# Kernel optimization log

Hardware: AMD Instinct MI355X
Metric: run time of the kernel (lower is better)

Reference implementation:

```python
import jax, jax.numpy as jnp
import numpy as np

N_NODES = 100000
N_EDGES = 1600000
D_IN = 128
D_OUT = 128
NEG_SLOPE = 0.01  # torch F.leaky_relu default


def setup_inputs() -> dict:
    key = jax.random.key(0)
    k1, k2, k3, k4, k5 = jax.random.split(key, 5)
    h = jax.random.normal(k1, (N_NODES, D_IN), dtype=jnp.float32)
    # nn.Linear default init scale ~ 1/sqrt(fan_in)
    W = jax.random.normal(k2, (D_IN, D_OUT), dtype=jnp.float32) / np.sqrt(D_IN)
    attn_w = jax.random.normal(k3, (2 * D_OUT,), dtype=jnp.float32) / np.sqrt(2 * D_OUT)
    edge_src = jax.random.randint(k4, (N_EDGES,), 0, N_NODES, dtype=jnp.int32)
    edge_dst = jax.random.randint(k5, (N_EDGES,), 0, N_NODES, dtype=jnp.int32)
    return {"h": h, "W": W, "attn_w": attn_w, "edge_src": edge_src, "edge_dst": edge_dst}


def reference(h, W, attn_w, edge_src, edge_dst):
    n = h.shape[0]
    d = W.shape[1]
    z = h @ W                                   # [N, d]
    # attention_func(cat([z_src, z_dst])) == z_src @ a[:d] + z_dst @ a[d:]
    s_src = z @ attn_w[:d]                      # [N]
    s_dst = z @ attn_w[d:]                      # [N]
    e = jax.nn.leaky_relu(s_src[edge_src] + s_dst[edge_dst], NEG_SLOPE)  # [E]
    # segment softmax over incoming edges of each dst node
    m = jax.ops.segment_max(e, edge_dst, num_segments=n)   # [N], -inf for empty
    ex = jnp.exp(e - m[edge_dst])                           # [E]
    denom = jax.ops.segment_sum(ex, edge_dst, num_segments=n)  # [N]
    alpha = ex / denom[edge_dst]                             # [E]
    # weighted neighbor sum: sum_j alpha_ij * z_j
    out = jax.ops.segment_sum(alpha[:, None] * z[edge_src], edge_dst, num_segments=n)
    return out
```

## Files before the change

kernel.cpp:

```cpp
#include <hip/hip_runtime.h>

#define D 128
#define NEG_SLOPE 0.01f
#define BSHIFT 7
#define B1 1024
#define SCHUNK 4096
#define SLOT 2560

typedef __attribute__((ext_vector_type(8))) short short8;
typedef __attribute__((ext_vector_type(4))) float floatx4;

__device__ __forceinline__ unsigned f2bf_rne(float x) {
    unsigned u = __float_as_uint(x);
    return (u + 0x7fffu + ((u >> 16) & 1u)) >> 16;
}
#define BF_LO(u) __uint_as_float((u) << 16)
#define BF_HI(u) __uint_as_float((u) & 0xffff0000u)

__global__ __launch_bounds__(256) void prep_wfrag(const float* __restrict__ W,
                                                  unsigned short* __restrict__ whi,
                                                  unsigned short* __restrict__ wlo,
                                                  int* __restrict__ gcur) {
    if (blockIdx.x == 0) {
        for (int i = threadIdx.x; i < B1; i += 256) gcur[i] = i * SLOT;
    }
    const int idx = blockIdx.x * 256 + threadIdx.x;
    const int j    = idx & 7;
    const int lane = (idx >> 3) & 63;
    const int tk   = idx >> 9;
    const int kk = tk & 3, ct = tk >> 2;
    const int k = kk * 32 + (lane >> 4) * 8 + j;
    const int n = ct * 16 + (lane & 15);
    const float x = W[k * D + n];
    const unsigned hi = f2bf_rne(x);
    const float hf = __uint_as_float(hi << 16);
    whi[idx] = (unsigned short)hi;
    wlo[idx] = (unsigned short)(__float_as_uint(x - hf) >> 16);
}

__global__ __launch_bounds__(1024) void sort_scatter(const int* __restrict__ esrc,
                                                     const int* __restrict__ edst,
                                                     int* __restrict__ gcur,
                                                     int* __restrict__ pairs, int E) {
    __shared__ int cnt[B1], exc[B1], gbs[B1], cur[B1];
    __shared__ int spk[SCHUNK];
    __shared__ unsigned short sbkt[SCHUNK];
    __shared__ int wtot[16];
    const int t = threadIdx.x;
    const int lane = t & 63, wv = t >> 6;
    cnt[t] = 0; cur[t] = 0;
    __syncthreads();

    const int e0 = blockIdx.x * SCHUNK;
    const int n  = min(SCHUNK, E - e0);

    int pk[4], bk[4];
    const int i0 = t * 4;
    if (i0 + 3 < n) {
        const int4 dv = *(const int4*)&edst[e0 + i0];
        const int4 sv = *(const int4*)&esrc[e0 + i0];
        const int dd[4] = {dv.x, dv.y, dv.z, dv.w};
        const int ss[4] = {sv.x, sv.y, sv.z, sv.w};
#pragma unroll
        for (int k = 0; k < 4; ++k) {
            bk[k] = dd[k] >> BSHIFT;
            pk[k] = (ss[k] << BSHIFT) | (dd[k] & 127);
            atomicAdd(&cnt[bk[k]], 1);
        }
    } else {
#pragma unroll
        for (int k = 0; k < 4; ++k) {
            const int i = i0 + k;
            if (i < n) {
                const int d = edst[e0 + i];
                const int s = esrc[e0 + i];
                bk[k] = d >> BSHIFT;
                pk[k] = (s << BSHIFT) | (d & 127);
                atomicAdd(&cnt[bk[k]], 1);
            } else {
                bk[k] = -1;
            }
        }
    }
    __syncthreads();

    const int c = cnt[t];
    int incl = c;
#pragma unroll
    for (int o = 1; o < 64; o <<= 1) {
        int v = __shfl_up(incl, o, 64);
        if (lane >= o) incl += v;
    }
    if (lane == 63) wtot[wv] = incl;
    __syncthreads();
    int wpre = 0;
#pragma unroll
    for (int i = 0; i < 16; ++i) wpre += (i < wv) ? wtot[i] : 0;
    exc[t] = wpre + incl - c;
    if (c > 0) gbs[t] = atomicAdd(&gcur[t], c);
    __syncthreads();

#pragma unroll
    for (int k = 0; k < 4; ++k) {
        if (bk[k] >= 0) {
            const int p = exc[bk[k]] + atomicAdd(&cur[bk[k]], 1);
            spk[p]  = pk[k];
            sbkt[p] = (unsigned short)bk[k];
        }
    }
    __syncthreads();

    for (int i = t; i < n; i += 1024) {
        const int b = sbkt[i];
        const int pos = gbs[b] + (i - exc[b]);
        if (pos < (b + 1) * SLOT) pairs[pos] = spk[i];
    }
}

__global__ __launch_bounds__(256) void fine_build(const int* __restrict__ pairs,
                                                  const int* __restrict__ gcur,
                                                  int* __restrict__ beg,
                                                  int* __restrict__ ncnt,
                                                  int* __restrict__ adj, int N) {
    __shared__ int cnt[4][128], woff[4][128], cur[4][128];
    __shared__ int sc[128];
    const int b = blockIdx.x;
    const int base = b << BSHIFT;
    const int nd = min(128, N - base);
    const int t = threadIdx.x;
    const int wv = t >> 6;
    const int s0 = b * SLOT;
    const int e1 = min(gcur[b], s0 + SLOT);
    for (int i = t; i < 512; i += 256) { (&cnt[0][0])[i] = 0; (&cur[0][0])[i] = 0; }
    __syncthreads();
    for (int i = s0 + t; i < e1; i += 256)
        atomicAdd(&cnt[wv][pairs[i] & 127], 1);
    __syncthreads();
    if (t < 128) {
        const int c0 = cnt[0][t], c1 = cnt[1][t], c2 = cnt[2][t];
        woff[0][t] = 0; woff[1][t] = c0; woff[2][t] = c0 + c1; woff[3][t] = c0 + c1 + c2;
        sc[t] = c0 + c1 + c2 + cnt[3][t];
    }
    __syncthreads();
    for (int off = 1; off < 128; off <<= 1) {
        int v = (t < 128 && t >= off) ? sc[t - off] : 0;
        __syncthreads();
        if (t < 128) sc[t] += v;
        __syncthreads();
    }
    if (t < 128) {
        const int tot = cnt[0][t] + cnt[1][t] + cnt[2][t] + cnt[3][t];
        const int excl = sc[t] - tot;
        if (t < nd) { beg[base + t] = s0 + excl; ncnt[base + t] = tot; }
        woff[0][t] += excl; woff[1][t] += excl; woff[2][t] += excl; woff[3][t] += excl;
    }
    __syncthreads();
    for (int i = s0 + t; i < e1; i += 256) {
        const int pkv = pairs[i];
        const int d = pkv & 127;
        const int pos = s0 + woff[wv][d] + atomicAdd(&cur[wv][d], 1);
        adj[pos] = pkv >> BSHIFT;
    }
}

__global__ __launch_bounds__(256, 3) void gemm_zs(const float* __restrict__ h,
                                                  const unsigned short* __restrict__ whi,
                                                  const unsigned short* __restrict__ wlo,
                                                  const float* __restrict__ aw,
                                                  unsigned short* __restrict__ z,
                                                  float* __restrict__ s_src,
                                                  float* __restrict__ s_dst, int N) {
    const int t = threadIdx.x;
    const int lane = t & 63, quad = lane >> 4, l16 = lane & 15;
    const int rowbase = blockIdx.x * 64 + (t >> 6) * 16;
    const int arow = min(rowbase + l16, N - 1);
    const float* __restrict__ hrow = h + (size_t)arow * D;

    float4 hx[8];
#pragma unroll
    for (int kk = 0; kk < 4; ++kk) {
        const int k0 = kk * 32 + quad * 8;
        hx[kk * 2]     = *(const float4*)&hrow[k0];
        hx[kk * 2 + 1] = *(const float4*)&hrow[k0 + 4];
    }
    union { short8 v; unsigned short u[8]; } ahi[4], alo[4];
#pragma unroll
    for (int kk = 0; kk < 4; ++kk) {
        const float xs[8] = {hx[kk*2].x, hx[kk*2].y, hx[kk*2].z, hx[kk*2].w,
                             hx[kk*2+1].x, hx[kk*2+1].y, hx[kk*2+1].z, hx[kk*2+1].w};
#pragma unroll
        for (int i = 0; i < 8; ++i) {
            const unsigned hi = f2bf_rne(xs[i]);
            const float hf = __uint_as_float(hi << 16);
            ahi[kk].u[i] = (unsigned short)hi;
            alo[kk].u[i] = (unsigned short)(__float_as_uint(xs[i] - hf) >> 16);
        }
    }

    floatx4 acc[8];
#pragma unroll
    for (int ct = 0; ct < 8; ++ct) acc[ct] = (floatx4){0.f, 0.f, 0.f, 0.f};

#pragma unroll
    for (int kk = 0; kk < 4; ++kk)
#pragma unroll
        for (int ct = 0; ct < 8; ++ct) {
            const int fo = ((ct * 4 + kk) * 64 + lane) * 8;
            short8 bhi = *(const short8*)&whi[fo];
            short8 blo = *(const short8*)&wlo[fo];
            acc[ct] = __builtin_amdgcn_mfma_f32_16x16x32_bf16(ahi[kk].v, bhi, acc[ct], 0, 0, 0);
            acc[ct] = __builtin_amdgcn_mfma_f32_16x16x32_bf16(alo[kk].v, bhi, acc[ct], 0, 0, 0);
            acc[ct] = __builtin_amdgcn_mfma_f32_16x16x32_bf16(ahi[kk].v, blo, acc[ct], 0, 0, 0);
        }

#pragma unroll
    for (int ct = 0; ct < 8; ++ct)
#pragma unroll
        for (int reg = 0; reg < 4; ++reg) {
            int r = rowbase + quad * 4 + reg;
            if (r < N)
                z[(size_t)r * D + ct * 16 + l16] = (unsigned short)f2bf_rne(acc[ct][reg]);
        }

    float ps[4] = {0.f, 0.f, 0.f, 0.f}, pd[4] = {0.f, 0.f, 0.f, 0.f};
#pragma unroll
    for (int ct = 0; ct < 8; ++ct) {
        float as = aw[ct * 16 + l16];
        float ad = aw[128 + ct * 16 + l16];
#pragma unroll
        for (int reg = 0; reg < 4; ++reg) {
            ps[reg] = fmaf(acc[ct][reg], as, ps[reg]);
            pd[reg] = fmaf(acc[ct][reg], ad, pd[reg]);
        }
    }
#pragma unroll
    for (int reg = 0; reg < 4; ++reg)
#pragma unroll
        for (int o = 1; o < 16; o <<= 1) {
            ps[reg] += __shfl_xor(ps[reg], o, 64);
            pd[reg] += __shfl_xor(pd[reg], o, 64);
        }
    if (l16 == 0) {
#pragma unroll
        for (int reg = 0; reg < 4; ++reg) {
            int r = rowbase + quad * 4 + reg;
            if (r < N) { s_src[r] = ps[reg]; s_dst[r] = pd[reg]; }
        }
    }
}

__global__ __launch_bounds__(256) void aggregate(const unsigned short* __restrict__ z,
                                                 const float* __restrict__ s_src,
                                                 const float* __restrict__ s_dst,
                                                 const int* __restrict__ beg_,
                                                 const int* __restrict__ ncnt_,
                                                 const int* __restrict__ adj,
                                                 float* __restrict__ out, int N) {
    const int lane = threadIdx.x & 63;
    const int half = lane >> 5;
    const int l32  = lane & 31;
    const int q2   = l32 >> 4;
    const int l16  = lane & 15;
    const int hb   = half << 5;
    const int pairBase = blockIdx.x * 8 + (threadIdx.x >> 6) * 2;
    if (pairBase >= N) return;
    const int nodeA = pairBase, nodeB = pairBase + 1;
    const int cA = ncnt_[nodeA], bA = beg_[nodeA];
    int cB = 0, bB = 0;
    if (nodeB < N) { cB = ncnt_[nodeB]; bB = beg_[nodeB]; }

    auto fma8 = [&](float* ac, float w, const uint4& v) {
        ac[0] = fmaf(w, BF_LO(v.x), ac[0]); ac[1] = fmaf(w, BF_HI(v.x), ac[1]);
        ac[2] = fmaf(w, BF_LO(v.y), ac[2]); ac[3] = fmaf(w, BF_HI(v.y), ac[3]);
        ac[4] = fmaf(w, BF_LO(v.z), ac[4]); ac[5] = fmaf(w, BF_HI(v.z), ac[5]);
        ac[6] = fmaf(w, BF_LO(v.w), ac[6]); ac[7] = fmaf(w, BF_HI(v.w), ac[7]);
    };

    if (max(cA, cB) <= 32) {
        const int myn = pairBase + half;
        const int mb  = half ? bB : bA;
        const int mc  = half ? cB : cA;
        const float sd = s_dst[myn < N ? myn : 0];
        int s = 0; float e = -INFINITY;
        if (l32 < mc) {
            s = adj[mb + l32];
            float tt = s_src[s] + sd;
            e = (tt >= 0.f) ? tt : NEG_SLOPE * tt;
        }
        int sj[4]; uint4 zv[4];
#pragma unroll
        for (int u = 0; u < 4; ++u) sj[u] = __shfl(s, hb + u * 2 + q2, 64);
#pragma unroll
        for (int u = 0; u < 4; ++u)
            zv[u] = *(const uint4*)&z[(size_t)sj[u] * D + l16 * 8];

        float mx = e;
#pragma unroll
        for (int o = 16; o; o >>= 1) mx = fmaxf(mx, __shfl_xor(mx, o, 64));
        float ex = (l32 < mc) ? __expf(e - mx) : 0.f;
        float sum = ex;
#pragma unroll
        for (int o = 16; o; o >>= 1) sum += __shfl_xor(sum, o, 64);
        const float inv = (mc > 0) ? 1.f / sum : 0.f;
        const float w = ex * inv;

        float a[8] = {0.f,0.f,0.f,0.f,0.f,0.f,0.f,0.f};
        float bacc[8] = {0.f,0.f,0.f,0.f,0.f,0.f,0.f,0.f};
#pragma unroll
        for (int u = 0; u < 4; ++u) {
            const int ji = u * 2 + q2;
            float wj = __shfl(w, hb + ji, 64);
            wj = (ji < mc) ? wj : 0.f;
            fma8((u & 1) ? bacc : a, wj, zv[u]);
        }
        for (int jj = 8; jj < mc; jj += 8) {
            int ji2[4]; float wj[4]; int sj2[4];
#pragma unroll
            for (int u = 0; u < 4; ++u) {
                ji2[u] = jj + u * 2 + q2;
                wj[u]  = __shfl(w, hb + ji2[u], 64);
                sj2[u] = __shfl(s, hb + ji2[u], 64);
                wj[u]  = (ji2[u] < mc) ? wj[u] : 0.f;
            }
            uint4 z0 = *(const uint4*)&z[(size_t)sj2[0] * D + l16 * 8];
            uint4 z1 = *(const uint4*)&z[(size_t)sj2[1] * D + l16 * 8];
            uint4 z2 = *(const uint4*)&z[(size_t)sj2[2] * D + l16 * 8];
            uint4 z3 = *(const uint4*)&z[(size_t)sj2[3] * D + l16 * 8];
            fma8(a, wj[0], z0);
            fma8(bacc, wj[1], z1);
            fma8(a, wj[2], z2);
            fma8(bacc, wj[3], z3);
        }
#pragma unroll
        for (int i = 0; i < 8; ++i) {
            a[i] += bacc[i];
            a[i] += __shfl_xor(a[i], 16, 64);
        }
        if (q2 == 0 && myn < N) {
            float* o = &out[(size_t)myn * D + l16 * 8];
            *(float4*)o       = make_float4(a[0], a[1], a[2], a[3]);
            *(float4*)(o + 4) = make_float4(a[4], a[5], a[6], a[7]);
        }
        return;
    }

    const int q = lane >> 4;
    for (int which = 0; which < 2; ++which) {
        const int myn = which ? nodeB : nodeA;
        if (myn >= N) break;
        const int mb = which ? bB : bA;
        const int mc = which ? cB : cA;
        const float sd = s_dst[myn];
        float a[8] = {0.f,0.f,0.f,0.f,0.f,0.f,0.f,0.f};
        float bacc[8] = {0.f,0.f,0.f,0.f,0.f,0.f,0.f,0.f};
        float mx = -INFINITY;
        for (int j = lane; j < mc; j += 64) {
            float tt = s_src[adj[mb + j]] + sd;
            tt = (tt >= 0.f) ? tt : NEG_SLOPE * tt;
            mx = fmaxf(mx, tt);
        }
#pragma unroll
        for (int o = 32; o; o >>= 1) mx = fmaxf(mx, __shfl_xor(mx, o, 64));
        float sum = 0.f;
        for (int j = lane; j < mc; j += 64) {
            float tt = s_src[adj[mb + j]] + sd;
            tt = (tt >= 0.f) ? tt : NEG_SLOPE * tt;
            sum += __expf(tt - mx);
        }
#pragma unroll
        for (int o = 32; o; o >>= 1) sum += __shfl_xor(sum, o, 64);
        const float inv = (mc > 0) ? 1.f / sum : 0.f;
        for (int base2 = 0; base2 < mc; base2 += 64) {
            const int cc = min(64, mc - base2);
            int s = 0; float w = 0.f;
            if (lane < cc) {
                s = adj[mb + base2 + lane];
                float tt = s_src[s] + sd;
                tt = (tt >= 0.f) ? tt : NEG_SLOPE * tt;
                w = __expf(tt - mx) * inv;
            }
            for (int jj = 0; jj < cc; jj += 8) {
                const int ja = jj + q;
                const int jb = ja + 4;
                float wa = __shfl(w, ja, 64); int sa = __shfl(s, ja, 64);
                float wb = __shfl(w, jb, 64); int sb = __shfl(s, jb, 64);
                wa = (ja < cc) ? wa : 0.f;
                wb = (jb < cc) ? wb : 0.f;
                uint4 za = *(const uint4*)&z[(size_t)sa * D + l16 * 8];
                uint4 zb = *(const uint4*)&z[(size_t)sb * D + l16 * 8];
                fma8(a, wa, za);
                fma8(bacc, wb, zb);
            }
        }
#pragma unroll
        for (int i = 0; i < 8; ++i) {
            a[i] += bacc[i];
            a[i] += __shfl_xor(a[i], 16, 64);
            a[i] += __shfl_xor(a[i], 32, 64);
        }
        if (q == 0) {
            float* o = &out[(size_t)myn * D + l16 * 8];
            *(float4*)o       = make_float4(a[0], a[1], a[2], a[3]);
            *(float4*)(o + 4) = make_float4(a[4], a[5], a[6], a[7]);
        }
    }
}

extern "C" void kernel_launch(void* const* d_in, const int* in_sizes, int n_in,
                              void* d_out, int out_size, void* d_ws, size_t ws_size,
                              hipStream_t stream) {
    const float* h    = (const float*)d_in[0];
    const float* W    = (const float*)d_in[1];
    const float* aw   = (const float*)d_in[2];
    const int*   esrc = (const int*)d_in[3];
    const int*   edst = (const int*)d_in[4];
    float* out = (float*)d_out;

    const int N = in_sizes[0] / D;
    const int E = in_sizes[3];
    const int NB1   = (N + 127) >> BSHIFT;
    const int NSORT = (E + SCHUNK - 1) / SCHUNK;

    char* p = (char*)d_ws;
    auto carve = [&](size_t bytes) {
        void* r = (void*)p;
        p += (bytes + 255) & ~size_t(255);
        return r;
    };
    unsigned short* z = (unsigned short*)carve(size_t(N) * D * sizeof(unsigned short));
    float* s_src  = (float*)carve(size_t(N) * sizeof(float));
    float* s_dst  = (float*)carve(size_t(N) * sizeof(float));
    int*   pairs  = (int*)carve(size_t(NB1) * SLOT * sizeof(int));
    int*   adj    = (int*)carve(size_t(NB1) * SLOT * sizeof(int));
    int*   beg    = (int*)carve(size_t(N) * sizeof(int));
    int*   ncnt   = (int*)carve(size_t(N) * sizeof(int));
    int*   gcur   = (int*)carve(size_t(B1) * sizeof(int));
    unsigned short* whi = (unsigned short*)carve(16384 * sizeof(unsigned short));
    unsigned short* wlo = (unsigned short*)carve(16384 * sizeof(unsigned short));
    (void)ws_size; (void)n_in; (void)out_size;

    prep_wfrag<<<64, 256, 0, stream>>>(W, whi, wlo, gcur);
    sort_scatter<<<NSORT, 1024, 0, stream>>>(esrc, edst, gcur, pairs, E);
    fine_build<<<NB1, 256, 0, stream>>>(pairs, gcur, beg, ncnt, adj, N);
    gemm_zs<<<(N + 63) / 64, 256, 0, stream>>>(h, whi, wlo, aw, z, s_src, s_dst, N);
    aggregate<<<(N + 7) / 8, 256, 0, stream>>>(z, s_src, s_dst, beg, ncnt, adj, out, N);
}
```

Measured before the change: 218.9 us.

## Fuse edge bucket sort and GEMM into one heterogeneous launch

Merges the coarse edge bucket-sort kernel and the z/score GEMM kernel into a single launch where the first blocks sort and the remaining blocks compute the GEMM, so the two independent phases overlap on the GPU and one launch gap disappears. Sort blocks shrink from 1024 to 256 threads, each handling 16 edges and a 4-bucket prefix scan. The risk is that GEMM blocks now carry the sort's large static LDS allocation, which may limit occupancy, and sort blocks do more serial work per thread.

```diff
diff --git a/kernel.cpp b/kernel.cpp
--- a/kernel.cpp
+++ b/kernel.cpp
@@ -5,6 +5,7 @@
 #define BSHIFT 7
 #define B1 1024
 #define SCHUNK 4096
+#define SEPT 16
 #define SLOT 2560
 
 typedef __attribute__((ext_vector_type(8))) short short8;
@@ -38,82 +39,182 @@
     wlo[idx] = (unsigned short)(__float_as_uint(x - hf) >> 16);
 }
 
-__global__ __launch_bounds__(1024) void sort_scatter(const int* __restrict__ esrc,
-                                                     const int* __restrict__ edst,
-                                                     int* __restrict__ gcur,
-                                                     int* __restrict__ pairs, int E) {
+__global__ __launch_bounds__(256, 3) void gemm_sort(
+        const int* __restrict__ esrc, const int* __restrict__ edst,
+        int* __restrict__ gcur, int* __restrict__ pairs, int E, int NSORT,
+        const float* __restrict__ h, const unsigned short* __restrict__ whi,
+        const unsigned short* __restrict__ wlo, const float* __restrict__ aw,
+        unsigned short* __restrict__ z, float* __restrict__ s_src,
+        float* __restrict__ s_dst, int N) {
     __shared__ int cnt[B1], exc[B1], gbs[B1], cur[B1];
     __shared__ int spk[SCHUNK];
     __shared__ unsigned short sbkt[SCHUNK];
-    __shared__ int wtot[16];
+    __shared__ int wtot[4];
     const int t = threadIdx.x;
-    const int lane = t & 63, wv = t >> 6;
-    cnt[t] = 0; cur[t] = 0;
-    __syncthreads();
-
-    const int e0 = blockIdx.x * SCHUNK;
-    const int n  = min(SCHUNK, E - e0);
-
-    int pk[4], bk[4];
-    const int i0 = t * 4;
-    if (i0 + 3 < n) {
-        const int4 dv = *(const int4*)&edst[e0 + i0];
-        const int4 sv = *(const int4*)&esrc[e0 + i0];
-        const int dd[4] = {dv.x, dv.y, dv.z, dv.w};
-        const int ss[4] = {sv.x, sv.y, sv.z, sv.w};
-#pragma unroll
-        for (int k = 0; k < 4; ++k) {
-            bk[k] = dd[k] >> BSHIFT;
-            pk[k] = (ss[k] << BSHIFT) | (dd[k] & 127);
-            atomicAdd(&cnt[bk[k]], 1);
-        }
-    } else {
-#pragma unroll
-        for (int k = 0; k < 4; ++k) {
-            const int i = i0 + k;
-            if (i < n) {
-                const int d = edst[e0 + i];
-                const int s = esrc[e0 + i];
-                bk[k] = d >> BSHIFT;
-                pk[k] = (s << BSHIFT) | (d & 127);
-                atomicAdd(&cnt[bk[k]], 1);
-            } else {
-                bk[k] = -1;
-            }
-        }
-    }
-    __syncthreads();
-
-    const int c = cnt[t];
-    int incl = c;
-#pragma unroll
-    for (int o = 1; o < 64; o <<= 1) {
-        int v = __shfl_up(incl, o, 64);
-        if (lane >= o) incl += v;
-    }
-    if (lane == 63) wtot[wv] = incl;
-    __syncthreads();
-    int wpre = 0;
-#pragma unroll
-    for (int i = 0; i < 16; ++i) wpre += (i < wv) ? wtot[i] : 0;
-    exc[t] = wpre + incl - c;
-    if (c > 0) gbs[t] = atomicAdd(&gcur[t], c);
-    __syncthreads();
-
-#pragma unroll
-    for (int k = 0; k < 4; ++k) {
-        if (bk[k] >= 0) {
-            const int p = exc[bk[k]] + atomicAdd(&cur[bk[k]], 1);
-            spk[p]  = pk[k];
-            sbkt[p] = (unsigned short)bk[k];
-        }
-    }
-    __syncthreads();
-
-    for (int i = t; i < n; i += 1024) {
-        const int b = sbkt[i];
-        const int pos = gbs[b] + (i - exc[b]);
-        if (pos < (b + 1) * SLOT) pairs[pos] = spk[i];
+    const int lane = t & 63;
+
+    if ((int)blockIdx.x < NSORT) {
+        const int wv = t >> 6;
+#pragma unroll
+        for (int k = 0; k < 4; ++k) { cnt[t + k * 256] = 0; cur[t + k * 256] = 0; }
+        __syncthreads();
+
+        const int e0 = blockIdx.x * SCHUNK;
+        const int n  = min(SCHUNK, E - e0);
+
+        int pk[SEPT], bk[SEPT];
+        const int i0 = t * SEPT;
+        if (i0 + SEPT - 1 < n) {
+#pragma unroll
+            for (int v4 = 0; v4 < 4; ++v4) {
+                const int4 dv = *(const int4*)&edst[e0 + i0 + v4 * 4];
+                const int4 sv = *(const int4*)&esrc[e0 + i0 + v4 * 4];
+                const int dd[4] = {dv.x, dv.y, dv.z, dv.w};
+                const int ss[4] = {sv.x, sv.y, sv.z, sv.w};
+#pragma unroll
+                for (int k = 0; k < 4; ++k) {
+                    const int kk2 = v4 * 4 + k;
+                    bk[kk2] = dd[k] >> BSHIFT;
+                    pk[kk2] = (ss[k] << BSHIFT) | (dd[k] & 127);
+                    atomicAdd(&cnt[bk[kk2]], 1);
+                }
+            }
+        } else {
+#pragma unroll
+            for (int k = 0; k < SEPT; ++k) {
+                const int i = i0 + k;
+                if (i < n) {
+                    const int d = edst[e0 + i];
+                    const int s = esrc[e0 + i];
+                    bk[k] = d >> BSHIFT;
+                    pk[k] = (s << BSHIFT) | (d & 127);
+                    atomicAdd(&cnt[bk[k]], 1);
+                } else {
+                    bk[k] = -1;
+                }
+            }
+        }
+        __syncthreads();
+
+        const int b0 = t << 2;
+        const int c0 = cnt[b0], c1 = cnt[b0 + 1], c2 = cnt[b0 + 2], c3 = cnt[b0 + 3];
+        const int s4 = c0 + c1 + c2 + c3;
+        int incl = s4;
+#pragma unroll
+        for (int o = 1; o < 64; o <<= 1) {
+            int v = __shfl_up(incl, o, 64);
+            if (lane >= o) incl += v;
+        }
+        if (lane == 63) wtot[wv] = incl;
+        __syncthreads();
+        int wpre = 0;
+#pragma unroll
+        for (int i = 0; i < 4; ++i) wpre += (i < wv) ? wtot[i] : 0;
+        const int ex0 = wpre + incl - s4;
+        exc[b0]     = ex0;
+        exc[b0 + 1] = ex0 + c0;
+        exc[b0 + 2] = ex0 + c0 + c1;
+        exc[b0 + 3] = ex0 + c0 + c1 + c2;
+        if (c0) gbs[b0]     = atomicAdd(&gcur[b0], c0);
+        if (c1) gbs[b0 + 1] = atomicAdd(&gcur[b0 + 1], c1);
+        if (c2) gbs[b0 + 2] = atomicAdd(&gcur[b0 + 2], c2);
+        if (c3) gbs[b0 + 3] = atomicAdd(&gcur[b0 + 3], c3);
+        __syncthreads();
+
+#pragma unroll
+        for (int k = 0; k < SEPT; ++k) {
+            if (bk[k] >= 0) {
+                const int p = exc[bk[k]] + atomicAdd(&cur[bk[k]], 1);
+                spk[p]  = pk[k];
+                sbkt[p] = (unsigned short)bk[k];
+            }
+        }
+        __syncthreads();
+
+        for (int i = t; i < n; i += 256) {
+            const int b = sbkt[i];
+            const int pos = gbs[b] + (i - exc[b]);
+            if (pos < (b + 1) * SLOT) pairs[pos] = spk[i];
+        }
+        return;
+    }
+
+    const int gbid = blockIdx.x - NSORT;
+    const int quad = lane >> 4, l16 = lane & 15;
+    const int rowbase = gbid * 64 + (t >> 6) * 16;
+    const int arow = min(rowbase + l16, N - 1);
+    const float* __restrict__ hrow = h + (size_t)arow * D;
+
+    float4 hx[8];
+#pragma unroll
+    for (int kk = 0; kk < 4; ++kk) {
+        const int k0 = kk * 32 + quad * 8;
+        hx[kk * 2]     = *(const float4*)&hrow[k0];
+        hx[kk * 2 + 1] = *(const float4*)&hrow[k0 + 4];
+    }
+    union { short8 v; unsigned short u[8]; } ahi[4], alo[4];
+#pragma unroll
+    for (int kk = 0; kk < 4; ++kk) {
+        const float xs[8] = {hx[kk*2].x, hx[kk*2].y, hx[kk*2].z, hx[kk*2].w,
+                             hx[kk*2+1].x, hx[kk*2+1].y, hx[kk*2+1].z, hx[kk*2+1].w};
+#pragma unroll
+        for (int i = 0; i < 8; ++i) {
+            const unsigned hi = f2bf_rne(xs[i]);
+            const float hf = __uint_as_float(hi << 16);
+            ahi[kk].u[i] = (unsigned short)hi;
+            alo[kk].u[i] = (unsigned short)(__float_as_uint(xs[i] - hf) >> 16);
+        }
+    }
+
+    floatx4 acc[8];
+#pragma unroll
+    for (int ct = 0; ct < 8; ++ct) acc[ct] = (floatx4){0.f, 0.f, 0.f, 0.f};
+
+#pragma unroll
+    for (int kk = 0; kk < 4; ++kk)
+#pragma unroll
+        for (int ct = 0; ct < 8; ++ct) {
+            const int fo = ((ct * 4 + kk) * 64 + lane) * 8;
+            short8 bhi = *(const short8*)&whi[fo];
+            short8 blo = *(const short8*)&wlo[fo];
+            acc[ct] = __builtin_amdgcn_mfma_f32_16x16x32_bf16(ahi[kk].v, bhi, acc[ct], 0, 0, 0);
+            acc[ct] = __builtin_amdgcn_mfma_f32_16x16x32_bf16(alo[kk].v, bhi, acc[ct], 0, 0, 0);
+            acc[ct] = __builtin_amdgcn_mfma_f32_16x16x32_bf16(ahi[kk].v, blo, acc[ct], 0, 0, 0);
+        }
+
+#pragma unroll
+    for (int ct = 0; ct < 8; ++ct)
+#pragma unroll
+        for (int reg = 0; reg < 4; ++reg) {
+            int r = rowbase + quad * 4 + reg;
+            if (r < N)
+                z[(size_t)r * D + ct * 16 + l16] = (unsigned short)f2bf_rne(acc[ct][reg]);
+        }
+
+    float ps[4] = {0.f, 0.f, 0.f, 0.f}, pd[4] = {0.f, 0.f, 0.f, 0.f};
+#pragma unroll
+    for (int ct = 0; ct < 8; ++ct) {
+        float as = aw[ct * 16 + l16];
+        float ad = aw[128 + ct * 16 + l16];
+#pragma unroll
+        for (int reg = 0; reg < 4; ++reg) {
+            ps[reg] = fmaf(acc[ct][reg], as, ps[reg]);
+            pd[reg] = fmaf(acc[ct][reg], ad, pd[reg]);
+        }
+    }
+#pragma unroll
+    for (int reg = 0; reg < 4; ++reg)
+#pragma unroll
+        for (int o = 1; o < 16; o <<= 1) {
+            ps[reg] += __shfl_xor(ps[reg], o, 64);
+            pd[reg] += __shfl_xor(pd[reg], o, 64);
+        }
+    if (l16 == 0) {
+#pragma unroll
+        for (int reg = 0; reg < 4; ++reg) {
+            int r = rowbase + quad * 4 + reg;
+            if (r < N) { s_src[r] = ps[reg]; s_dst[r] = pd[reg]; }
+        }
     }
 }
 
@@ -163,92 +264,6 @@
     }
 }
 
-__global__ __launch_bounds__(256, 3) void gemm_zs(const float* __restrict__ h,
-                                                  const unsigned short* __restrict__ whi,
-                                                  const unsigned short* __restrict__ wlo,
-                                                  const float* __restrict__ aw,
-                                                  unsigned short* __restrict__ z,
-                                                  float* __restrict__ s_src,
-                                                  float* __restrict__ s_dst, int N) {
-    const int t = threadIdx.x;
-    const int lane = t & 63, quad = lane >> 4, l16 = lane & 15;
-    const int rowbase = blockIdx.x * 64 + (t >> 6) * 16;
-    const int arow = min(rowbase + l16, N - 1);
-    const float* __restrict__ hrow = h + (size_t)arow * D;
-
-    float4 hx[8];
-#pragma unroll
-    for (int kk = 0; kk < 4; ++kk) {
-        const int k0 = kk * 32 + quad * 8;
-        hx[kk * 2]     = *(const float4*)&hrow[k0];
-        hx[kk * 2 + 1] = *(const float4*)&hrow[k0 + 4];
-    }
-    union { short8 v; unsigned short u[8]; } ahi[4], alo[4];
-#pragma unroll
-    for (int kk = 0; kk < 4; ++kk) {
-        const float xs[8] = {hx[kk*2].x, hx[kk*2].y, hx[kk*2].z, hx[kk*2].w,
-                             hx[kk*2+1].x, hx[kk*2+1].y, hx[kk*2+1].z, hx[kk*2+1].w};
-#pragma unroll
-        for (int i = 0; i < 8; ++i) {
-            const unsigned hi = f2bf_rne(xs[i]);
-            const float hf = __uint_as_float(hi << 16);
-            ahi[kk].u[i] = (unsigned short)hi;
-            alo[kk].u[i] = (unsigned short)(__float_as_uint(xs[i] - hf) >> 16);
-        }
-    }
-
-    floatx4 acc[8];
-#pragma unroll
-    for (int ct = 0; ct < 8; ++ct) acc[ct] = (floatx4){0.f, 0.f, 0.f, 0.f};
-
-#pragma unroll
-    for (int kk = 0; kk < 4; ++kk)
-#pragma unroll
-        for (int ct = 0; ct < 8; ++ct) {
-            const int fo = ((ct * 4 + kk) * 64 + lane) * 8;
-            short8 bhi = *(const short8*)&whi[fo];
-            short8 blo = *(const short8*)&wlo[fo];
-            acc[ct] = __builtin_amdgcn_mfma_f32_16x16x32_bf16(ahi[kk].v, bhi, acc[ct], 0, 0, 0);
-            acc[ct] = __builtin_amdgcn_mfma_f32_16x16x32_bf16(alo[kk].v, bhi, acc[ct], 0, 0, 0);
-            acc[ct] = __builtin_amdgcn_mfma_f32_16x16x32_bf16(ahi[kk].v, blo, acc[ct], 0, 0, 0);
-        }
-
-#pragma unroll
-    for (int ct = 0; ct < 8; ++ct)
-#pragma unroll
-        for (int reg = 0; reg < 4; ++reg) {
-            int r = rowbase + quad * 4 + reg;
-            if (r < N)
-                z[(size_t)r * D + ct * 16 + l16] = (unsigned short)f2bf_rne(acc[ct][reg]);
-        }
-
-    float ps[4] = {0.f, 0.f, 0.f, 0.f}, pd[4] = {0.f, 0.f, 0.f, 0.f};
-#pragma unroll
-    for (int ct = 0; ct < 8; ++ct) {
-        float as = aw[ct * 16 + l16];
-        float ad = aw[128 + ct * 16 + l16];
-#pragma unroll
-        for (int reg = 0; reg < 4; ++reg) {
-            ps[reg] = fmaf(acc[ct][reg], as, ps[reg]);
-            pd[reg] = fmaf(acc[ct][reg], ad, pd[reg]);
-        }
-    }
-#pragma unroll
-    for (int reg = 0; reg < 4; ++reg)
-#pragma unroll
-        for (int o = 1; o < 16; o <<= 1) {
-            ps[reg] += __shfl_xor(ps[reg], o, 64);
-            pd[reg] += __shfl_xor(pd[reg], o, 64);
-        }
-    if (l16 == 0) {
-#pragma unroll
-        for (int reg = 0; reg < 4; ++reg) {
-            int r = rowbase + quad * 4 + reg;
-            if (r < N) { s_src[r] = ps[reg]; s_dst[r] = pd[reg]; }
-        }
-    }
-}
-
 __global__ __launch_bounds__(256) void aggregate(const unsigned short* __restrict__ z,
                                                  const float* __restrict__ s_src,
                                                  const float* __restrict__ s_dst,
@@ -420,6 +435,7 @@
     const int E = in_sizes[3];
     const int NB1   = (N + 127) >> BSHIFT;
     const int NSORT = (E + SCHUNK - 1) / SCHUNK;
+    const int NGEMM = (N + 63) / 64;
 
     char* p = (char*)d_ws;
     auto carve = [&](size_t bytes) {
@@ -440,8 +456,8 @@
     (void)ws_size; (void)n_in; (void)out_size;
 
     prep_wfrag<<<64, 256, 0, stream>>>(W, whi, wlo, gcur);
-    sort_scatter<<<NSORT, 1024, 0, stream>>>(esrc, edst, gcur, pairs, E);
+    gemm_sort<<<NSORT + NGEMM, 256, 0, stream>>>(esrc, edst, gcur, pairs, E, NSORT,
+                                                 h, whi, wlo, aw, z, s_src, s_dst, N);
     fine_build<<<NB1, 256, 0, stream>>>(pairs, gcur, beg, ncnt, adj, N);
-    gemm_zs<<<(N + 63) / 64, 256, 0, stream>>>(h, whi, wlo, aw, z, s_src, s_dst, N);
     aggregate<<<(N + 7) / 8, 256, 0, stream>>>(z, s_src, s_dst, beg, ncnt, adj, out, N);
 }
```

After: 234.2 us. 1.07x slower.
